# Optimization experiments

Hardware: AMD Instinct MI355X
Metric: run time of the kernel (lower is better)

## Reference

```python
import jax, jax.numpy as jnp
import numpy as np

M, IN_F, OUT_F = 32, 8192, 32768
ACT_QMAX = 127.0  # act_bits=8


def unpack_int4(w_packed, in_features):
    # w_packed: (out, in//2) int32 holding two int4 nibbles per byte
    lower = w_packed & 15
    upper = (w_packed >> 4) & 15
    # sign-extend 4-bit values: v - ((v & 8) << 1) maps 8..15 -> -8..-1
    lower = lower - ((lower & 8) << 1)
    upper = upper - ((upper & 8) << 1)
    w = jnp.stack([lower, upper], axis=-1).reshape(w_packed.shape[0], -1)
    return w[:, :in_features]


def setup_inputs() -> dict:
    key = jax.random.key(0)
    k1, k2, k3, k4, k5 = jax.random.split(key, 5)
    x = jax.random.normal(k1, (M, IN_F), dtype=jnp.float32)
    # random packed bytes in [0, 256): every value is a valid pair of int4 nibbles
    weight_packed = jax.random.randint(k2, (OUT_F, IN_F // 2), 0, 256, dtype=jnp.int32)
    weight_scale = jax.random.uniform(k3, (OUT_F, 1), dtype=jnp.float32) * 0.01 + 1e-4
    act_scale = jax.random.uniform(k4, (1,), dtype=jnp.float32) * 0.1 + 0.01
    bias = jax.random.normal(k5, (OUT_F,), dtype=jnp.float32)
    return {"x": x, "weight_packed": weight_packed, "weight_scale": weight_scale,
            "act_scale": act_scale, "bias": bias}


def reference(x, weight_packed, weight_scale, act_scale, bias):
    # 1) static input quantization (round + clamp to int8 range, kept in fp32)
    x_q = jnp.clip(jnp.round(x / act_scale), -ACT_QMAX, ACT_QMAX)
    # 2) unpack int4 weights and emulate GEMM in fp32 (as the original does)
    w = unpack_int4(weight_packed, x.shape[-1]).astype(jnp.float32)  # (out, in)
    y_q = jnp.einsum('mi,oi->mo', x_q, w)  # (M, out)
    # 3) dequant: act_scale * per-channel weight_scale, then bias
    y = y_q * (act_scale * weight_scale.T)  # weight_scale.T: (1, out)
    y = y + bias[None, :]
    return y
```

## Files before the change

kernel.cpp:

```cpp
#include <hip/hip_runtime.h>
#include <stdint.h>


#define M_DIM  32
#define IN_FEAT 8192
#define OUT_FEAT 32768
#define KSPLIT 4
#define KSLICE (IN_FEAT / KSPLIT)
#define NITER  (KSLICE / 64)

typedef __attribute__((ext_vector_type(4))) int   i32x4;
typedef __attribute__((ext_vector_type(4))) float f32x4;

__global__ __launch_bounds__(256) void quant_kernel(
    const float* __restrict__ x,
    const float* __restrict__ act_scale,
    int* __restrict__ xq4) {
  int i = blockIdx.x * blockDim.x + threadIdx.x;
  float s = act_scale[0];
  f32x4 v = ((const f32x4*)x)[i];
  int r = 0;
#pragma unroll
  for (int j = 0; j < 4; ++j) {
    float q = rintf(v[j] / s);
    q = fminf(fmaxf(q, -127.0f), 127.0f);
    r |= ((int)q & 0xFF) << (8 * j);
  }
  xq4[i] = r;
}

__device__ __forceinline__ int unpack2(int v) {
  return ((v << 4) | (v << 8)) & 0xF0F0;
}

__global__ __launch_bounds__(256) void gemm_kernel(
    const char* __restrict__ xq,
    const int*  __restrict__ wp,
    int* __restrict__ partial)
{
  const int lane = threadIdx.x & 63;
  const int wave = threadIdx.x >> 6;
  const int l15  = lane & 15;
  const int krow = lane >> 4;

  const int kslice = blockIdx.x & (KSPLIT - 1);
  const int nblk   = blockIdx.x >> 2;
  const int n      = (nblk << 6) + (wave << 4) + l15;
  const int kbase  = kslice * KSLICE;

  const i32x4* a0p = (const i32x4*)(xq + (size_t)l15        * IN_FEAT + kbase);
  const i32x4* a1p = (const i32x4*)(xq + (size_t)(l15 + 16) * IN_FEAT + kbase);
  const i32x4* bp  = (const i32x4*)((const char*)(wp + (size_t)n * (IN_FEAT / 2))
                                    + (size_t)kbase * 2);

  i32x4 acc0 = {0, 0, 0, 0};
  i32x4 acc1 = {0, 0, 0, 0};

  i32x4 w_lo = __builtin_nontemporal_load(&bp[krow * 2]);
  i32x4 w_hi = __builtin_nontemporal_load(&bp[krow * 2 + 1]);
  i32x4 a0   = a0p[krow];
  i32x4 a1   = a1p[krow];

#pragma unroll 2
  for (int i = 0; i < NITER; ++i) {
    const int ip = (i + 1 < NITER) ? (i + 1) : (NITER - 1);
    i32x4 w_lo_n = __builtin_nontemporal_load(&bp[ip * 8 + krow * 2]);
    i32x4 w_hi_n = __builtin_nontemporal_load(&bp[ip * 8 + krow * 2 + 1]);
    i32x4 a0_n   = a0p[ip * 4 + krow];
    i32x4 a1_n   = a1p[ip * 4 + krow];

    int p0 = unpack2(w_lo[0]);
    int p1 = unpack2(w_lo[1]);
    int p2 = unpack2(w_lo[2]);
    int p3 = unpack2(w_lo[3]);
    int p4 = unpack2(w_hi[0]);
    int p5 = unpack2(w_hi[1]);
    int p6 = unpack2(w_hi[2]);
    int p7 = unpack2(w_hi[3]);
    i32x4 bfrag;
    bfrag[0] = __builtin_amdgcn_perm(p1, p0, 0x05040100);
    bfrag[1] = __builtin_amdgcn_perm(p3, p2, 0x05040100);
    bfrag[2] = __builtin_amdgcn_perm(p5, p4, 0x05040100);
    bfrag[3] = __builtin_amdgcn_perm(p7, p6, 0x05040100);

    acc0 = __builtin_amdgcn_mfma_i32_16x16x64_i8(a0, bfrag, acc0, 0, 0, 0);
    acc1 = __builtin_amdgcn_mfma_i32_16x16x64_i8(a1, bfrag, acc1, 0, 0, 0);

    w_lo = w_lo_n; w_hi = w_hi_n; a0 = a0_n; a1 = a1_n;
  }

  int* pout = partial + (size_t)kslice * (M_DIM * OUT_FEAT);
  const int m0 = krow * 4;
#pragma unroll
  for (int r = 0; r < 4; ++r) {
    __builtin_nontemporal_store(acc0[r], &pout[(size_t)(m0 + r)      * OUT_FEAT + n]);
    __builtin_nontemporal_store(acc1[r], &pout[(size_t)(m0 + r + 16) * OUT_FEAT + n]);
  }
}

__global__ __launch_bounds__(256) void reduce_kernel(
    const int*   __restrict__ partial,
    const float* __restrict__ wscale,
    const float* __restrict__ act_scale,
    const float* __restrict__ bias,
    float* __restrict__ out)
{
  const int t  = blockIdx.x * blockDim.x + threadIdx.x;
  const int m  = t >> 13;
  const int n4 = (t & 8191) << 2;
  const size_t off = (size_t)m * OUT_FEAT + n4;

  i32x4 s = *(const i32x4*)(partial + off);
#pragma unroll
  for (int k = 1; k < KSPLIT; ++k)
    s += *(const i32x4*)(partial + (size_t)k * (M_DIM * OUT_FEAT) + off);

  const float as = act_scale[0] * (1.0f / 16.0f);
  f32x4 ws = *(const f32x4*)(wscale + n4);
  f32x4 bs = *(const f32x4*)(bias + n4);
  f32x4 r;
#pragma unroll
  for (int j = 0; j < 4; ++j)
    r[j] = (float)s[j] * (as * ws[j]) + bs[j];
  *(f32x4*)(out + off) = r;
}

extern "C" void kernel_launch(void* const* d_in, const int* in_sizes, int n_in,
                              void* d_out, int out_size, void* d_ws, size_t ws_size,
                              hipStream_t stream) {
  const float* x      = (const float*)d_in[0];
  const int*   wp     = (const int*)  d_in[1];
  const float* wscale = (const float*)d_in[2];
  const float* ascale = (const float*)d_in[3];
  const float* bias   = (const float*)d_in[4];
  float* out = (float*)d_out;

  int*  partial = (int*)d_ws;
  char* xq      = (char*)d_ws + (size_t)KSPLIT * M_DIM * OUT_FEAT * sizeof(int);

  quant_kernel<<<(M_DIM * IN_FEAT / 4) / 256, 256, 0, stream>>>(x, ascale, (int*)xq);
  gemm_kernel<<<(OUT_FEAT / 64) * KSPLIT, 256, 0, stream>>>(xq, wp, partial);
  reduce_kernel<<<(M_DIM * OUT_FEAT / 4) / 256, 256, 0, stream>>>(partial, wscale, ascale, bias, out);
}
```

Baseline: 730.2 us.

## Permute quantized activation layout to simplify int4 weight unpacking in GEMM

The quantize kernel now writes int8 activations in a permuted order within each 64-element block, so the K ordering matches a cheaper weight-unpack pattern. In the GEMM, each lane gathers the low bytes of four packed int32 words into one register and splits the nibbles with two masks and perm instructions, replacing eight per-word unpack calls. The per-lane weight load offsets change to match. This lowers ALU work per MFMA. The cost is a scattered-store layout in the quant kernel, and correctness depends on the activation and weight K orders staying consistent.

Measured after the change: 713.9 us. 2.2% less time.

```diff
diff --git a/kernel.cpp b/kernel.cpp
--- a/kernel.cpp
+++ b/kernel.cpp
@@ -15,22 +15,29 @@
 __global__ __launch_bounds__(256) void quant_kernel(
     const float* __restrict__ x,
     const float* __restrict__ act_scale,
-    int* __restrict__ xq4) {
-  int i = blockIdx.x * blockDim.x + threadIdx.x;
-  float s = act_scale[0];
-  f32x4 v = ((const f32x4*)x)[i];
-  int r = 0;
+    char* __restrict__ xq) {
+  const int t  = blockIdx.x * blockDim.x + threadIdx.x;
+  const int m  = t >> 10;
+  const int g8 = t & 1023;
+  const int k0 = g8 << 3;
+  const int blk = k0 >> 6;
+  const int g   = (k0 >> 3) & 7;
+  const int pos = blk * 64 + ((g < 4) ? g * 16 : (g - 4) * 16 + 8);
+
+  const float s = act_scale[0];
+  const f32x4 v0 = *(const f32x4*)(x + (size_t)m * IN_FEAT + k0);
+  const f32x4 v1 = *(const f32x4*)(x + (size_t)m * IN_FEAT + k0 + 4);
+  int r0 = 0, r1 = 0;
 #pragma unroll
   for (int j = 0; j < 4; ++j) {
-    float q = rintf(v[j] / s);
-    q = fminf(fmaxf(q, -127.0f), 127.0f);
-    r |= ((int)q & 0xFF) << (8 * j);
+    float qa = fminf(fmaxf(rintf(v0[j] / s), -127.0f), 127.0f);
+    float qb = fminf(fmaxf(rintf(v1[j] / s), -127.0f), 127.0f);
+    r0 |= ((int)qa & 0xFF) << (8 * j);
+    r1 |= ((int)qb & 0xFF) << (8 * j);
   }
-  xq4[i] = r;
-}
-
-__device__ __forceinline__ int unpack2(int v) {
-  return ((v << 4) | (v << 8)) & 0xF0F0;
+  int* dst = (int*)(xq + (size_t)m * IN_FEAT + pos);
+  dst[0] = r0;
+  dst[1] = r1;
 }
 
 __global__ __launch_bounds__(256) void gemm_kernel(
@@ -56,32 +63,30 @@
   i32x4 acc0 = {0, 0, 0, 0};
   i32x4 acc1 = {0, 0, 0, 0};
 
-  i32x4 w_lo = __builtin_nontemporal_load(&bp[krow * 2]);
-  i32x4 w_hi = __builtin_nontemporal_load(&bp[krow * 2 + 1]);
+  i32x4 w_lo = __builtin_nontemporal_load(&bp[krow]);
+  i32x4 w_hi = __builtin_nontemporal_load(&bp[4 + krow]);
   i32x4 a0   = a0p[krow];
   i32x4 a1   = a1p[krow];
 
 #pragma unroll 2
   for (int i = 0; i < NITER; ++i) {
     const int ip = (i + 1 < NITER) ? (i + 1) : (NITER - 1);
-    i32x4 w_lo_n = __builtin_nontemporal_load(&bp[ip * 8 + krow * 2]);
-    i32x4 w_hi_n = __builtin_nontemporal_load(&bp[ip * 8 + krow * 2 + 1]);
+    i32x4 w_lo_n = __builtin_nontemporal_load(&bp[ip * 8 + krow]);
+    i32x4 w_hi_n = __builtin_nontemporal_load(&bp[ip * 8 + 4 + krow]);
     i32x4 a0_n   = a0p[ip * 4 + krow];
     i32x4 a1_n   = a1p[ip * 4 + krow];
 
-    int p0 = unpack2(w_lo[0]);
-    int p1 = unpack2(w_lo[1]);
-    int p2 = unpack2(w_lo[2]);
-    int p3 = unpack2(w_lo[3]);
-    int p4 = unpack2(w_hi[0]);
-    int p5 = unpack2(w_hi[1]);
-    int p6 = unpack2(w_hi[2]);
-    int p7 = unpack2(w_hi[3]);
+    int b0  = w_lo[0] | (w_lo[1] << 8) | (w_lo[2] << 16) | (w_lo[3] << 24);
+    int b1  = w_hi[0] | (w_hi[1] << 8) | (w_hi[2] << 16) | (w_hi[3] << 24);
+    int lo0 = (b0 << 4) & 0xF0F0F0F0;
+    int hi0 =  b0       & 0xF0F0F0F0;
+    int lo1 = (b1 << 4) & 0xF0F0F0F0;
+    int hi1 =  b1       & 0xF0F0F0F0;
     i32x4 bfrag;
-    bfrag[0] = __builtin_amdgcn_perm(p1, p0, 0x05040100);
-    bfrag[1] = __builtin_amdgcn_perm(p3, p2, 0x05040100);
-    bfrag[2] = __builtin_amdgcn_perm(p5, p4, 0x05040100);
-    bfrag[3] = __builtin_amdgcn_perm(p7, p6, 0x05040100);
+    bfrag[0] = __builtin_amdgcn_perm(hi0, lo0, 0x05010400);
+    bfrag[1] = __builtin_amdgcn_perm(hi0, lo0, 0x07030602);
+    bfrag[2] = __builtin_amdgcn_perm(hi1, lo1, 0x05010400);
+    bfrag[3] = __builtin_amdgcn_perm(hi1, lo1, 0x07030602);
 
     acc0 = __builtin_amdgcn_mfma_i32_16x16x64_i8(a0, bfrag, acc0, 0, 0, 0);
     acc1 = __builtin_amdgcn_mfma_i32_16x16x64_i8(a1, bfrag, acc1, 0, 0, 0);
@@ -138,7 +143,7 @@
   int*  partial = (int*)d_ws;
   char* xq      = (char*)d_ws + (size_t)KSPLIT * M_DIM * OUT_FEAT * sizeof(int);
 
-  quant_kernel<<<(M_DIM * IN_FEAT / 4) / 256, 256, 0, stream>>>(x, ascale, (int*)xq);
+  quant_kernel<<<(M_DIM * IN_FEAT / 8) / 256, 256, 0, stream>>>(x, ascale, xq);
   gemm_kernel<<<(OUT_FEAT / 64) * KSPLIT, 256, 0, stream>>>(xq, wp, partial);
   reduce_kernel<<<(M_DIM * OUT_FEAT / 4) / 256, 256, 0, stream>>>(partial, wscale, ascale, bias, out);
 }
```
